# Kernel optimization log

Hardware: AMD Instinct MI355X
Metric: run time of the kernel (lower is better)

Reference implementation:

```python
import jax, jax.numpy as jnp
import numpy as np

BN_EPS = 1e-5

def setup_inputs() -> dict:
    key = jax.random.key(0)
    k1, k2, k3 = jax.random.split(key, 3)
    B, C, H, W = 8, 96, 56, 56
    Cout = 2 * C  # must equal 2*C for the BatchNorm in the original module
    x = jax.random.normal(k1, (B, C, H, W), dtype=jnp.float32)
    conv_w = jax.random.normal(k2, (Cout, 2 * C), dtype=jnp.float32) * (1.0 / np.sqrt(2 * C))
    conv_b = jax.random.normal(k3, (Cout,), dtype=jnp.float32) * 0.01
    gamma = jnp.ones((Cout,), dtype=jnp.float32)
    beta = jnp.zeros((Cout,), dtype=jnp.float32)
    return {"x": x, "conv_w": conv_w, "conv_b": conv_b, "gamma": gamma, "beta": beta}

def _forward(x, conv_w, conv_b, gamma, beta):
    B, C, H, W = x.shape
    # b c h w -> b n c, n = H*W
    q = x.reshape(B, C, H * W).transpose(0, 2, 1)
    # unscaled self-attention (q == k == v == tokens)
    att = jnp.einsum('bnc,bmc->bnm', q, q)          # [B, N, N]
    att = jax.nn.softmax(att, axis=-1)
    att = jnp.einsum('bnm,bmc->bnc', att, q)        # [B, N, C]
    att = att.transpose(0, 2, 1).reshape(B, C, H, W)
    # max-relative: x_j = max(0, x - att) since x_j starts at zeros
    x_j = jnp.maximum(x - att, 0.0)
    cat = jnp.concatenate([x, x_j], axis=1)          # [B, 2C, H, W]
    # 1x1 conv
    y = jnp.einsum('bchw,oc->bohw', cat, conv_w) + conv_b[None, :, None, None]
    # BatchNorm2d in training mode: biased batch stats over (B, H, W)
    mean = jnp.mean(y, axis=(0, 2, 3), keepdims=True)
    var = jnp.var(y, axis=(0, 2, 3), keepdims=True)
    y = (y - mean) * jax.lax.rsqrt(var + BN_EPS)
    y = y * gamma[None, :, None, None] + beta[None, :, None, None]
    # torch nn.GELU default is exact (erf) GELU
    return jax.nn.gelu(y, approximate=False)

def reference(x, conv_w, conv_b, gamma, beta):
    return _forward(x, conv_w, conv_b, gamma, beta)
```

## Files before the change

### kernel.cpp

```cpp
#include <hip/hip_runtime.h>
#include <hip/hip_bf16.h>

#define B_    8
#define C_    96
#define N_    3136
#define COUT_ 192
#define NTOK_ 25088
#define BN_EPS 1e-5f

#define CROW 200
#define BNC  (B_ * N_ * C_)
#define NSPLIT 4
#define NT98  98

#define K2_KL_OFF 7168
#define K2_V_OFF  14336
#define K2_BUFSZ  22528

typedef __hip_bfloat16 bf16;
typedef unsigned short u16;
typedef unsigned int u32;
typedef __attribute__((ext_vector_type(8))) short short8;
typedef __attribute__((ext_vector_type(16))) float f32x16;

__device__ __forceinline__ u16 f2bf(float f) {
    union { __hip_bfloat16 h; u16 u; } cv;
    cv.h = __float2bfloat16(f);
    return cv.u;
}
__device__ __forceinline__ float bf2f(u16 v) {
    union { u16 u; __hip_bfloat16 h; } cv;
    cv.u = v;
    return __bfloat162float(cv.h);
}
__device__ __forceinline__ u32 packbf2(float lo, float hi) {
    return ((u32)f2bf(hi) << 16) | (u32)f2bf(lo);
}

__device__ __forceinline__ void gload_lds16(const void* g, void* l) {
    __builtin_amdgcn_global_load_lds((const __attribute__((address_space(1))) void*)g,
                                     (__attribute__((address_space(3))) void*)l,
                                     16, 0, 0);
}

__global__ __launch_bounds__(256) void transpose_split(const float* __restrict__ x,
                                                       u16* __restrict__ xt_hi,
                                                       u16* __restrict__ xt_lo,
                                                       u16* __restrict__ xc_hi,
                                                       float* __restrict__ norm2) {
    __shared__ float tile[32][33];
    __shared__ float nrm[32];
    const int nb = blockIdx.x * 32;
    const int cb = blockIdx.y * 32;
    const int b  = blockIdx.z;
    const int tid = threadIdx.x;
    const int tx = tid & 31;
    const int ty = tid >> 5;
    if (tid < 32) nrm[tid] = 0.0f;
    float psum = 0.0f;
#pragma unroll
    for (int r = 0; r < 32; r += 8) {
        size_t idx = ((size_t)b * C_ + cb + ty + r) * N_ + nb + tx;
        float v = x[idx];
        tile[ty + r][tx] = v;
        xc_hi[idx] = f2bf(v);
        psum = fmaf(v, v, psum);
    }
    __syncthreads();
    atomicAdd(&nrm[tx], psum);
#pragma unroll
    for (int it = 0; it < 4; it++) {
        const int n2 = (tid >> 4) + it * 16;
        const int cp = tid & 15;
        float v0 = tile[2 * cp][n2];
        float v1 = tile[2 * cp + 1][n2];
        u16 h0 = f2bf(v0), h1 = f2bf(v1);
        u16 l0 = f2bf(v0 - bf2f(h0)), l1 = f2bf(v1 - bf2f(h1));
        size_t o = ((size_t)b * N_ + nb + n2) * C_ + cb + 2 * cp;
        *(u32*)&xt_hi[o] = (u32)h0 | ((u32)h1 << 16);
        *(u32*)&xt_lo[o] = (u32)l0 | ((u32)l1 << 16);
        if (it == 1) break;
    }
    __syncthreads();
    if (tid < 32)
        atomicAdd(&norm2[(size_t)b * N_ + nb + tid], nrm[tid]);
}

__global__ __launch_bounds__(256) void cast_w(const float* __restrict__ w,
                                              u16* __restrict__ whi,
                                              u16* __restrict__ wlo) {
    int i = blockIdx.x * 256 + threadIdx.x;
    if (i >= COUT_ * 2 * C_) return;
    float v = w[i];
    u16 h = f2bf(v);
    whi[i] = h;
    wlo[i] = f2bf(v - bf2f(h));
}

__global__ __launch_bounds__(256) void norm_max(const float* __restrict__ norm2,
                                                int* __restrict__ maxbits) {
    const int tid = threadIdx.x;
    float m = 0.0f;
    for (int i = tid; i < NTOK_; i += 256) m = fmaxf(m, norm2[i]);
#pragma unroll
    for (int d = 1; d < 64; d <<= 1) m = fmaxf(m, __shfl_xor(m, d));
    __shared__ float wmax[4];
    if ((tid & 63) == 0) wmax[tid >> 6] = m;
    __syncthreads();
    if (tid == 0) {
        float mm = fmaxf(fmaxf(wmax[0], wmax[1]), fmaxf(wmax[2], wmax[3]));
        *maxbits = __float_as_int(mm);
    }
}

__global__ __launch_bounds__(256, 3) void flash_attn_mfma32(const u16* __restrict__ xt_hi,
                                                            const u16* __restrict__ xt_lo,
                                                            const u16* __restrict__ xc_hi,
                                                            const float* __restrict__ norm2,
                                                            const int* __restrict__ maxbits,
                                                            float* __restrict__ attT,
                                                            float* __restrict__ l_arr) {
    __shared__ __align__(16) char LDSU[2][K2_BUFSZ];
    const int b     = blockIdx.y;
    const int i0    = blockIdx.x * 128;
    const int split = blockIdx.z;
    const int kt0   = (NT98 * split) / NSPLIT;
    const int kt1   = (NT98 * (split + 1)) / NSPLIT;
    const int tid   = threadIdx.x;
    const int lane  = tid & 63;
    const int w     = tid >> 6;
    const int col   = lane & 31;
    const int g     = lane >> 5;

    const u16* th = xt_hi + (size_t)b * N_ * C_;
    const u16* tl = xt_lo + (size_t)b * N_ * C_;
    const u16* vh = xc_hi + (size_t)b * C_ * N_;

    u32 loff[6], dofs[6];
#pragma unroll
    for (int j = 0; j < 6; j++) {
        int s = w + 4 * j;
        if (s >= 22) { loff[j] = 0; dofs[j] = 0; continue; }
        if (s < 14) {
            int kind = s < 7 ? 0 : 1;
            int t = s - kind * 7;
            int p = t * 64 + lane;
            int r = p / 13, c = p % 13;
            if (c > 11) c = 11;
            loff[j] = (r < 32) ? (u32)(r * 192 + c * 16) : 0u;
            dofs[j] = (u32)(kind * K2_KL_OFF + t * 1024);
        } else {
            int t = s - 14;
            int p = t * 64 + lane;
            int ch = p / 5, c = p % 5;
            if (c > 3) c = 3;
            loff[j] = (ch < 96) ? (u32)(ch * (N_ * 2) + c * 16) : 0u;
            dofs[j] = (u32)(K2_V_OFF + t * 1024);
        }
    }

    const int qrow  = i0 + w * 32 + col;
    const int qrowc = qrow < N_ ? qrow : N_ - 1;
    short8 qh[6], ql[6];
#pragma unroll
    for (int kc = 0; kc < 6; kc++) {
        qh[kc] = *(const short8*)&th[(size_t)qrowc * C_ + kc * 16 + g * 8];
        ql[kc] = *(const short8*)&tl[(size_t)qrowc * C_ + kc * 16 + g * 8];
    }
    const float maxn2 = __int_as_float(*maxbits);
    const float m_i   = sqrtf(norm2[(size_t)b * N_ + qrowc] * maxn2);
    float l_acc = 0.0f;
    f32x16 O0 = {0}, O1 = {0}, O2 = {0};

    auto stage = [&](int nbuf, int kt) {
        const u32 ktK = (u32)kt * 6144u;
        const u32 ktV = (u32)kt * 64u;
#pragma unroll
        for (int j = 0; j < 6; j++) {
            int s = w + 4 * j;
            if (s >= 22) break;
            const char* sb = (s < 7)  ? (const char*)th + ktK
                           : (s < 14) ? (const char*)tl + ktK
                                      : (const char*)vh + ktV;
            gload_lds16(sb + loff[j], (char*)&LDSU[nbuf][0] + dofs[j]);
        }
    };

    stage(0, kt0);
    __syncthreads();

    const int g16 = g * 16;
    int buf = 0;
    for (int kt = kt0; kt < kt1; kt++) {
        if (kt + 1 < kt1) stage(buf ^ 1, kt + 1);

        const char* Lb = (const char*)&LDSU[buf][0];

        f32x16 S = {0};
        __builtin_amdgcn_s_setprio(1);
#pragma unroll
        for (int kc = 0; kc < 6; kc++) {
            const int o2 = col * 208 + kc * 32 + g16;
            short8 kh = *(const short8*)(Lb + o2);
            short8 kl = *(const short8*)(Lb + K2_KL_OFF + o2);
            S = __builtin_amdgcn_mfma_f32_32x32x16_bf16(kh, ql[kc], S, 0, 0, 0);
            S = __builtin_amdgcn_mfma_f32_32x32x16_bf16(kl, qh[kc], S, 0, 0, 0);
            S = __builtin_amdgcn_mfma_f32_32x32x16_bf16(kh, qh[kc], S, 0, 0, 0);
        }
        __builtin_amdgcn_s_setprio(0);

        float p[16];
#pragma unroll
        for (int r = 0; r < 16; r++) {
            p[r] = __expf(S[r] - m_i);
            l_acc += p[r];
        }
        u32 w8[8];
#pragma unroll
        for (int q = 0; q < 8; q++) w8[q] = packbf2(p[2 * q], p[2 * q + 1]);

        __builtin_amdgcn_s_setprio(1);
#pragma unroll
        for (int kc = 0; kc < 2; kc++) {
            const int qb = kc * 4;
            u32 a0 = w8[qb + 0], a1 = w8[qb + 1];
            u32 a2 = w8[qb + 2], a3 = w8[qb + 3];
            u32 s0 = __shfl_xor((int)a0, 32), s1 = __shfl_xor((int)a1, 32);
            u32 s2 = __shfl_xor((int)a2, 32), s3 = __shfl_xor((int)a3, 32);
            union { short8 v; u32 u[4]; } Bf;
            Bf.u[0] = g ? s2 : a0;
            Bf.u[1] = g ? s3 : a1;
            Bf.u[2] = g ? a2 : s0;
            Bf.u[3] = g ? a3 : s1;
            const int vo = K2_V_OFF + col * 80 + kc * 32 + g16;
            short8 v0 = *(const short8*)(Lb + vo);
            short8 v1 = *(const short8*)(Lb + vo + 2560);
            short8 v2 = *(const short8*)(Lb + vo + 5120);
            O0 = __builtin_amdgcn_mfma_f32_32x32x16_bf16(v0, Bf.v, O0, 0, 0, 0);
            O1 = __builtin_amdgcn_mfma_f32_32x32x16_bf16(v1, Bf.v, O1, 0, 0, 0);
            O2 = __builtin_amdgcn_mfma_f32_32x32x16_bf16(v2, Bf.v, O2, 0, 0, 0);
        }
        __builtin_amdgcn_s_setprio(0);

        __syncthreads();
        buf ^= 1;
    }

    if (qrow < N_) {
        float* ab = attT + (size_t)b * C_ * N_ + qrow;
#pragma unroll
        for (int r = 0; r < 16; r++) {
            int c = (r & 3) + 8 * (r >> 2) + 4 * g;
            atomicAdd(&ab[(size_t)(c)      * N_], O0[r]);
            atomicAdd(&ab[(size_t)(c + 32) * N_], O1[r]);
            atomicAdd(&ab[(size_t)(c + 64) * N_], O2[r]);
        }
        float l_tot = l_acc + __shfl_xor(l_acc, 32);
        if (g == 0) atomicAdd(&l_arr[(size_t)b * N_ + qrow], l_tot);
    }
}

__global__ __launch_bounds__(128, 3) void conv_mfma(const float* __restrict__ x,
                                                    const float* __restrict__ attT,
                                                    const float* __restrict__ l_arr,
                                                    const u16* __restrict__ whi,
                                                    const u16* __restrict__ wlo,
                                                    const float* __restrict__ convb,
                                                    float* __restrict__ y) {
    __shared__ u16 ch[32 * CROW];
    __shared__ u16 cl[32 * CROW];
    __shared__ float invl[32];
    const int b   = blockIdx.x / (N_ / 32);
    const int n0  = (blockIdx.x % (N_ / 32)) * 32;
    const int tid = threadIdx.x;

    if (tid < 32) invl[tid] = 1.0f / l_arr[(size_t)b * N_ + n0 + tid];
    __syncthreads();

    const float* xb = x    + (size_t)b * C_ * N_ + n0;
    const float* ab = attT + (size_t)b * C_ * N_ + n0;
    for (int e = tid; e < 32 * C_; e += 128) {
        int c = e >> 5, t = e & 31;
        float xv = xb[(size_t)c * N_ + t];
        float au = ab[(size_t)c * N_ + t];
        float xj = fmaxf(xv - au * invl[t], 0.0f);
        u16 h1 = f2bf(xv);
        ch[t * CROW + c] = h1;
        cl[t * CROW + c] = f2bf(xv - bf2f(h1));
        u16 h2 = f2bf(xj);
        ch[t * CROW + C_ + c] = h2;
        cl[t * CROW + C_ + c] = f2bf(xj - bf2f(h2));
    }
    __syncthreads();

    const int lane = tid & 63;
    const int w    = tid >> 6;
    const int col  = lane & 31;
    const int g    = lane >> 5;
    const int m0   = w * 3;

    f32x16 A[3] = {{0}, {0}, {0}};
#pragma unroll
    for (int ks = 0; ks < 12; ks++) {
        const int k0 = ks * 16;
        short8 bh = *(const short8*)&ch[col * CROW + k0 + g * 8];
        short8 bl = *(const short8*)&cl[col * CROW + k0 + g * 8];
#pragma unroll
        for (int mt = 0; mt < 3; mt++) {
            const size_t wo = (size_t)((m0 + mt) * 32 + col) * (2 * C_) + k0 + g * 8;
            short8 ah = *(const short8*)&whi[wo];
            short8 al = *(const short8*)&wlo[wo];
            A[mt] = __builtin_amdgcn_mfma_f32_32x32x16_bf16(ah, bl, A[mt], 0, 0, 0);
            A[mt] = __builtin_amdgcn_mfma_f32_32x32x16_bf16(al, bh, A[mt], 0, 0, 0);
            A[mt] = __builtin_amdgcn_mfma_f32_32x32x16_bf16(ah, bh, A[mt], 0, 0, 0);
        }
    }

    float* yb = y + (size_t)b * COUT_ * N_ + n0 + col;
#pragma unroll
    for (int mt = 0; mt < 3; mt++)
#pragma unroll
        for (int r = 0; r < 16; r++) {
            int o = (m0 + mt) * 32 + (r & 3) + 8 * (r >> 2) + 4 * g;
            yb[(size_t)o * N_] = A[mt][r] + convb[o];
        }
}

__global__ __launch_bounds__(256) void bn_partial(const float* __restrict__ y,
                                                  float* __restrict__ pb) {
    const int o   = blockIdx.x;
    const int b   = blockIdx.y;
    const int tid = threadIdx.x;
    float s = 0.0f, q = 0.0f;
    const float4* p = (const float4*)(y + (size_t)(b * COUT_ + o) * N_);
    for (int i = tid; i < N_ / 4; i += 256) {
        float4 v = p[i];
        s += v.x + v.y + v.z + v.w;
        q += v.x * v.x + v.y * v.y + v.z * v.z + v.w * v.w;
    }
#pragma unroll
    for (int d = 1; d < 64; d <<= 1) {
        s += __shfl_xor(s, d);
        q += __shfl_xor(q, d);
    }
    __shared__ float wss[4], wqq[4];
    if ((tid & 63) == 0) { wss[tid >> 6] = s; wqq[tid >> 6] = q; }
    __syncthreads();
    if (tid == 0) {
        pb[b * COUT_ + o]                = wss[0] + wss[1] + wss[2] + wss[3];
        pb[B_ * COUT_ + b * COUT_ + o]   = wqq[0] + wqq[1] + wqq[2] + wqq[3];
    }
}

__global__ __launch_bounds__(192) void bn_finish(const float* __restrict__ pb,
                                                 const float* __restrict__ gamma,
                                                 const float* __restrict__ beta,
                                                 float* __restrict__ ss) {
    const int o = threadIdx.x;
    float s = 0.0f, q = 0.0f;
#pragma unroll
    for (int b = 0; b < B_; b++) {
        s += pb[b * COUT_ + o];
        q += pb[B_ * COUT_ + b * COUT_ + o];
    }
    const float invn = 1.0f / (float)NTOK_;
    float mean = s * invn;
    float var  = q * invn - mean * mean;
    float sc   = gamma[o] * rsqrtf(var + BN_EPS);
    ss[o]         = sc;
    ss[COUT_ + o] = beta[o] - mean * sc;
}

__global__ __launch_bounds__(256) void bn_gelu_out(const float* __restrict__ y,
                                                   const float* __restrict__ ss,
                                                   float* __restrict__ out) {
    const int total4 = (B_ * COUT_ * N_) / 4;
    int i = blockIdx.x * 256 + threadIdx.x;
    if (i >= total4) return;
    int base = i * 4;
    int o = (base / N_) % COUT_;
    float sc = ss[o], sh = ss[COUT_ + o];
    float4 v = *(const float4*)&y[base];
    float u0 = fmaf(v.x, sc, sh), u1 = fmaf(v.y, sc, sh);
    float u2 = fmaf(v.z, sc, sh), u3 = fmaf(v.w, sc, sh);
    const float k = 0.70710678118654752f;
    float4 g;
    g.x = 0.5f * u0 * (1.0f + erff(u0 * k));
    g.y = 0.5f * u1 * (1.0f + erff(u1 * k));
    g.z = 0.5f * u2 * (1.0f + erff(u2 * k));
    g.w = 0.5f * u3 * (1.0f + erff(u3 * k));
    *(float4*)&out[base] = g;
}

extern "C" void kernel_launch(void* const* d_in, const int* in_sizes, int n_in,
                              void* d_out, int out_size, void* d_ws, size_t ws_size,
                              hipStream_t stream) {
    const float* x     = (const float*)d_in[0];
    const float* w     = (const float*)d_in[1];
    const float* cb    = (const float*)d_in[2];
    const float* gamma = (const float*)d_in[3];
    const float* beta  = (const float*)d_in[4];

    u16* xt_hi = (u16*)d_ws;
    u16* xt_lo = xt_hi + (size_t)BNC;
    u16* xc_hi = xt_lo + (size_t)BNC;
    float* attT  = (float*)(xc_hi + (size_t)BNC);
    u16* whi   = (u16*)(attT + (size_t)BNC);
    u16* wlo   = whi + COUT_ * 2 * C_;
    float* y     = (float*)(wlo + COUT_ * 2 * C_);
    float* ss    = y + (size_t)B_ * COUT_ * N_;
    float* l_arr = ss + 2 * COUT_;
    float* norm2 = l_arr + NTOK_;
    int*   maxb  = (int*)(norm2 + NTOK_);
    float* pb    = attT;

    hipMemsetAsync(l_arr, 0, NTOK_ * sizeof(float), stream);
    hipMemsetAsync(norm2, 0, NTOK_ * sizeof(float), stream);
    hipMemsetAsync(attT, 0, (size_t)BNC * sizeof(float), stream);

    transpose_split<<<dim3(N_ / 32, C_ / 32, B_), 256, 0, stream>>>(x, xt_hi, xt_lo, xc_hi, norm2);
    cast_w<<<dim3((COUT_ * 2 * C_ + 255) / 256), 256, 0, stream>>>(w, whi, wlo);
    norm_max<<<dim3(1), 256, 0, stream>>>(norm2, maxb);
    flash_attn_mfma32<<<dim3((N_ + 127) / 128, B_, NSPLIT), 256, 0, stream>>>(
        xt_hi, xt_lo, xc_hi, norm2, maxb, attT, l_arr);
    conv_mfma<<<dim3(B_ * (N_ / 32)), 128, 0, stream>>>(x, attT, l_arr, whi, wlo, cb, y);
    bn_partial<<<dim3(COUT_, B_), 256, 0, stream>>>(y, pb);
    bn_finish<<<dim3(1), 192, 0, stream>>>(pb, gamma, beta, ss);
    bn_gelu_out<<<dim3((B_ * COUT_ * N_ / 4 + 255) / 256), 256, 0, stream>>>(y, ss, (float*)d_out);
}
```

Before: 238.4 us.

## Load V fragments directly from global memory and parallelize norm max reduction

The attention kernel stops staging V tiles into LDS and instead loads the V MFMA operands straight from global memory (L2/L1) into registers each iteration. This shrinks the LDS buffer from 22.5KB to 14KB per stage and removes the V async copies. The cost is exposed global-load latency that is no longer double-buffered. The norm max reduction now runs over 25 blocks with an atomicMax on float bits, which needs a new memset of the result. The transpose loop is also tidied to two iterations without the early break.

```diff
diff --git a/kernel.cpp b/kernel.cpp
--- a/kernel.cpp
+++ b/kernel.cpp
@@ -14,8 +14,7 @@
 #define NT98  98
 
 #define K2_KL_OFF 7168
-#define K2_V_OFF  14336
-#define K2_BUFSZ  22528
+#define K2_BUFSZ  14336
 
 typedef __hip_bfloat16 bf16;
 typedef unsigned short u16;
@@ -69,7 +68,7 @@
     __syncthreads();
     atomicAdd(&nrm[tx], psum);
 #pragma unroll
-    for (int it = 0; it < 4; it++) {
+    for (int it = 0; it < 2; it++) {
         const int n2 = (tid >> 4) + it * 16;
         const int cp = tid & 15;
         float v0 = tile[2 * cp][n2];
@@ -79,7 +78,6 @@
         size_t o = ((size_t)b * N_ + nb + n2) * C_ + cb + 2 * cp;
         *(u32*)&xt_hi[o] = (u32)h0 | ((u32)h1 << 16);
         *(u32*)&xt_lo[o] = (u32)l0 | ((u32)l1 << 16);
-        if (it == 1) break;
     }
     __syncthreads();
     if (tid < 32)
@@ -99,18 +97,12 @@
 
 __global__ __launch_bounds__(256) void norm_max(const float* __restrict__ norm2,
                                                 int* __restrict__ maxbits) {
-    const int tid = threadIdx.x;
+    const int tid = blockIdx.x * 256 + threadIdx.x;
     float m = 0.0f;
-    for (int i = tid; i < NTOK_; i += 256) m = fmaxf(m, norm2[i]);
+    for (int i = tid; i < NTOK_; i += gridDim.x * 256) m = fmaxf(m, norm2[i]);
 #pragma unroll
     for (int d = 1; d < 64; d <<= 1) m = fmaxf(m, __shfl_xor(m, d));
-    __shared__ float wmax[4];
-    if ((tid & 63) == 0) wmax[tid >> 6] = m;
-    __syncthreads();
-    if (tid == 0) {
-        float mm = fmaxf(fmaxf(wmax[0], wmax[1]), fmaxf(wmax[2], wmax[3]));
-        *maxbits = __float_as_int(mm);
-    }
+    if ((threadIdx.x & 63) == 0) atomicMax(maxbits, __float_as_int(m));
 }
 
 __global__ __launch_bounds__(256, 3) void flash_attn_mfma32(const u16* __restrict__ xt_hi,
@@ -136,27 +128,18 @@
     const u16* tl = xt_lo + (size_t)b * N_ * C_;
     const u16* vh = xc_hi + (size_t)b * C_ * N_;
 
-    u32 loff[6], dofs[6];
-#pragma unroll
-    for (int j = 0; j < 6; j++) {
+    u32 loff[4], dofs[4];
+#pragma unroll
+    for (int j = 0; j < 4; j++) {
         int s = w + 4 * j;
-        if (s >= 22) { loff[j] = 0; dofs[j] = 0; continue; }
-        if (s < 14) {
-            int kind = s < 7 ? 0 : 1;
-            int t = s - kind * 7;
-            int p = t * 64 + lane;
-            int r = p / 13, c = p % 13;
-            if (c > 11) c = 11;
-            loff[j] = (r < 32) ? (u32)(r * 192 + c * 16) : 0u;
-            dofs[j] = (u32)(kind * K2_KL_OFF + t * 1024);
-        } else {
-            int t = s - 14;
-            int p = t * 64 + lane;
-            int ch = p / 5, c = p % 5;
-            if (c > 3) c = 3;
-            loff[j] = (ch < 96) ? (u32)(ch * (N_ * 2) + c * 16) : 0u;
-            dofs[j] = (u32)(K2_V_OFF + t * 1024);
-        }
+        if (s >= 14) { loff[j] = 0; dofs[j] = 0; continue; }
+        int kind = s < 7 ? 0 : 1;
+        int t = s - kind * 7;
+        int p = t * 64 + lane;
+        int r = p / 13, c = p % 13;
+        if (c > 11) c = 11;
+        loff[j] = (r < 32) ? (u32)(r * 192 + c * 16) : 0u;
+        dofs[j] = (u32)(kind * K2_KL_OFF + t * 1024);
     }
 
     const int qrow  = i0 + w * 32 + col;
@@ -174,14 +157,12 @@
 
     auto stage = [&](int nbuf, int kt) {
         const u32 ktK = (u32)kt * 6144u;
-        const u32 ktV = (u32)kt * 64u;
-#pragma unroll
-        for (int j = 0; j < 6; j++) {
+#pragma unroll
+        for (int j = 0; j < 4; j++) {
             int s = w + 4 * j;
-            if (s >= 22) break;
-            const char* sb = (s < 7)  ? (const char*)th + ktK
-                           : (s < 14) ? (const char*)tl + ktK
-                                      : (const char*)vh + ktV;
+            if (s >= 14) break;
+            const char* sb = (s < 7) ? (const char*)th + ktK
+                                     : (const char*)tl + ktK;
             gload_lds16(sb + loff[j], (char*)&LDSU[nbuf][0] + dofs[j]);
         }
     };
@@ -192,7 +173,16 @@
     const int g16 = g * 16;
     int buf = 0;
     for (int kt = kt0; kt < kt1; kt++) {
+        const int n0 = kt * 64 / 2;
         if (kt + 1 < kt1) stage(buf ^ 1, kt + 1);
+
+        short8 vf[6];
+#pragma unroll
+        for (int kc = 0; kc < 2; kc++)
+#pragma unroll
+            for (int j = 0; j < 3; j++)
+                vf[kc * 3 + j] = *(const short8*)&vh[(size_t)(32 * j + col) * N_ +
+                                                     kt * 32 + kc * 16 + g * 8];
 
         const char* Lb = (const char*)&LDSU[buf][0];
 
@@ -232,13 +222,9 @@
             Bf.u[1] = g ? s3 : a1;
             Bf.u[2] = g ? a2 : s0;
             Bf.u[3] = g ? a3 : s1;
-            const int vo = K2_V_OFF + col * 80 + kc * 32 + g16;
-            short8 v0 = *(const short8*)(Lb + vo);
-            short8 v1 = *(const short8*)(Lb + vo + 2560);
-            short8 v2 = *(const short8*)(Lb + vo + 5120);
-            O0 = __builtin_amdgcn_mfma_f32_32x32x16_bf16(v0, Bf.v, O0, 0, 0, 0);
-            O1 = __builtin_amdgcn_mfma_f32_32x32x16_bf16(v1, Bf.v, O1, 0, 0, 0);
-            O2 = __builtin_amdgcn_mfma_f32_32x32x16_bf16(v2, Bf.v, O2, 0, 0, 0);
+            O0 = __builtin_amdgcn_mfma_f32_32x32x16_bf16(vf[kc * 3 + 0], Bf.v, O0, 0, 0, 0);
+            O1 = __builtin_amdgcn_mfma_f32_32x32x16_bf16(vf[kc * 3 + 1], Bf.v, O1, 0, 0, 0);
+            O2 = __builtin_amdgcn_mfma_f32_32x32x16_bf16(vf[kc * 3 + 2], Bf.v, O2, 0, 0, 0);
         }
         __builtin_amdgcn_s_setprio(0);
 
@@ -416,11 +402,12 @@
 
     hipMemsetAsync(l_arr, 0, NTOK_ * sizeof(float), stream);
     hipMemsetAsync(norm2, 0, NTOK_ * sizeof(float), stream);
+    hipMemsetAsync(maxb, 0, sizeof(int), stream);
     hipMemsetAsync(attT, 0, (size_t)BNC * sizeof(float), stream);
 
     transpose_split<<<dim3(N_ / 32, C_ / 32, B_), 256, 0, stream>>>(x, xt_hi, xt_lo, xc_hi, norm2);
     cast_w<<<dim3((COUT_ * 2 * C_ + 255) / 256), 256, 0, stream>>>(w, whi, wlo);
-    norm_max<<<dim3(1), 256, 0, stream>>>(norm2, maxb);
+    norm_max<<<dim3(25), 256, 0, stream>>>(norm2, maxb);
     flash_attn_mfma32<<<dim3((N_ + 127) / 128, B_, NSPLIT), 256, 0, stream>>>(
         xt_hi, xt_lo, xc_hi, norm2, maxb, attT, l_arr);
     conv_mfma<<<dim3(B_ * (N_ / 32)), 128, 0, stream>>>(x, attT, l_arr, whi, wlo, cb, y);
```

After: 237.3 us. No clear change (-0.4%).
